# Optimization experiments

Hardware: AMD Instinct MI355X
Metric: run time of the kernel (lower is better)

Reference implementation:

```python
import jax, jax.numpy as jnp
import numpy as np

N_NODES = 100000
N_EDGES = 1000000
M_DIM = 4
HID = 64
N_GRAPHS = 64


def setup_inputs() -> dict:
    key = jax.random.key(0)
    ks = jax.random.split(key, 16)
    x = jax.random.normal(ks[0], (N_NODES, 1, M_DIM), dtype=jnp.float32)
    edge_index = jax.random.randint(ks[1], (2, N_EDGES), 0, N_NODES, dtype=jnp.int64)
    batch = jnp.sort(jax.random.randint(ks[2], (N_NODES,), 0, N_GRAPHS, dtype=jnp.int64))
    def lin(k, out_c, in_c):
        bound = 1.0 / np.sqrt(in_c)
        return jax.random.uniform(k, (out_c, in_c), jnp.float32, -bound, bound)
    inp = {"x": x, "edge_index": edge_index, "batch": batch}
    inp["W1l"] = lin(ks[3], HID, 1); inp["b1l"] = jnp.zeros((HID,), jnp.float32)
    inp["W1r"] = lin(ks[4], HID, 1)
    inp["W2l"] = lin(ks[5], HID, HID); inp["b2l"] = jnp.zeros((HID,), jnp.float32)
    inp["W2r"] = lin(ks[6], HID, HID)
    inp["W3l"] = lin(ks[7], HID, HID); inp["b3l"] = jnp.zeros((HID,), jnp.float32)
    inp["W3r"] = lin(ks[8], HID, HID)
    inp["Wlin"] = lin(ks[9], 1, HID); inp["blin"] = jnp.zeros((1,), jnp.float32)
    return inp


def _sage_conv(x, src, dst, Wl, bl, Wr):
    # x: [N, F, M]; mean aggregation over in-edges, then lin_l/lin_r GEMMs.
    N, F, M = x.shape
    msg = x[src]  # [E, F, M] gather
    s = jax.ops.segment_sum(msg, dst, num_segments=N)
    cnt = jax.ops.segment_sum(jnp.ones((src.shape[0],), x.dtype), dst, num_segments=N)
    agg = s / jnp.maximum(cnt, 1.0)[:, None, None]  # [N, F, M]
    C = Wl.shape[0]
    # torch .view(N*M, F) on contiguous [N,F,M] == row-major reshape (mixes F and M)
    h = (agg.reshape(N * M, F) @ Wl.T + bl).reshape(N, C, M)
    h = h + (x.reshape(N * M, F) @ Wr.T).reshape(N, C, M)
    return h


def reference(x, edge_index, batch, W1l, b1l, W1r, W2l, b2l, W2r, W3l, b3l, W3r, Wlin, blin):
    src, dst = edge_index[0], edge_index[1]
    h = jax.nn.relu(_sage_conv(x, src, dst, W1l, b1l, W1r))
    h = jax.nn.relu(_sage_conv(h, src, dst, W2l, b2l, W2r))
    h = jax.nn.relu(_sage_conv(h, src, dst, W3l, b3l, W3r))
    # new_global_mean_pool: scatter-mean over nodes -> [B, HID, M]
    sums = jax.ops.segment_sum(h, batch, num_segments=N_GRAPHS)
    cnts = jax.ops.segment_sum(jnp.ones((h.shape[0],), h.dtype), batch, num_segments=N_GRAPHS)
    pooled = sums / jnp.maximum(cnts, 1.0)[:, None, None]
    # dropout in eval mode == identity
    B, F, M = pooled.shape
    z = (pooled.reshape(B * M, F) @ Wlin.T + blin).reshape(B, M)
    return jax.nn.sigmoid(z).mean(axis=1)  # [B]
```

## Files before the change

### kernel.cpp

```cpp
#include <hip/hip_runtime.h>
#include <math.h>

#define TPB 256

typedef unsigned short ushort_t;
typedef unsigned char uchar_t;
typedef __attribute__((ext_vector_type(8))) short short8v;
typedef __attribute__((ext_vector_type(4))) float f32x4;
typedef __attribute__((ext_vector_type(8))) unsigned short ushort8;

__device__ __forceinline__ unsigned short f2b(float f) {
  union { float f; unsigned int i; } c; c.f = f;
  unsigned int x = c.i;
  x += 0x7FFFu + ((x >> 16) & 1u);
  return (unsigned short)(x >> 16);
}
__device__ __forceinline__ float b2f(unsigned short u) {
  union { unsigned int i; float f; } c; c.i = ((unsigned int)u) << 16; return c.f;
}

__device__ __forceinline__ short8v fp8x8_to_bf16(const uchar_t* p) {
  uint2 u = *(const uint2*)p;
  auto p0 = __builtin_amdgcn_cvt_pk_f32_fp8(u.x, false);
  auto p1 = __builtin_amdgcn_cvt_pk_f32_fp8(u.x, true);
  auto p2 = __builtin_amdgcn_cvt_pk_f32_fp8(u.y, false);
  auto p3 = __builtin_amdgcn_cvt_pk_f32_fp8(u.y, true);
  ushort8 o;
  o[0] = f2b(p0[0]); o[1] = f2b(p0[1]); o[2] = f2b(p1[0]); o[3] = f2b(p1[1]);
  o[4] = f2b(p2[0]); o[5] = f2b(p2[1]); o[6] = f2b(p3[0]); o[7] = f2b(p3[1]);
  union { ushort8 a; short8v b; } c; c.a = o; return c.b;
}

__global__ void k_histg(const int* __restrict__ dst, int* deg,
                        const int* __restrict__ batch, int* gcnt, int E, int N) {
  int t = blockIdx.x * TPB + threadIdx.x;
  if (t < E) atomicAdd(&deg[dst[t]], 1);
  int n0 = t * 16;
  if (n0 < N) {
    int n1 = min(n0 + 16, N);
    int cur = batch[n0];
    int c = 0;
    for (int n = n0; n < n1; ++n) {
      int b = batch[n];
      if (b != cur) { atomicAdd(&gcnt[cur], c); cur = b; c = 0; }
      ++c;
    }
    atomicAdd(&gcnt[cur], c);
  }
}

__global__ void k_scan1(const int* __restrict__ deg, int* rp, int* bsum, int N) {
  __shared__ int s[TPB];
  int t = threadIdx.x;
  int i = blockIdx.x * TPB + t;
  int v = (i < N) ? ((deg[i] + 7) & ~7) : 0;
  s[t] = v;
  __syncthreads();
  for (int d = 1; d < TPB; d <<= 1) {
    int u = (t >= d) ? s[t - d] : 0;
    __syncthreads();
    s[t] += u;
    __syncthreads();
  }
  if (i < N) rp[i] = s[t] - v;
  if (t == TPB - 1) bsum[blockIdx.x] = s[t];
}

__global__ void k_scan2(const int* bsum, int* boff, int nb) {
  __shared__ int s[1024];
  int t = threadIdx.x;
  int v = (t < nb) ? bsum[t] : 0;
  s[t] = v;
  __syncthreads();
  for (int d = 1; d < 1024; d <<= 1) {
    int u = (t >= d) ? s[t - d] : 0;
    __syncthreads();
    s[t] += u;
    __syncthreads();
  }
  if (t < nb) boff[t] = s[t] - v;
}

__global__ void k_scan3(int* rp, const int* __restrict__ boff, const int* __restrict__ bsum,
                        int* cursor, int N, int nb) {
  int i = blockIdx.x * TPB + threadIdx.x;
  if (i < N) {
    int v = rp[i] + boff[i >> 8];
    rp[i] = v;
    cursor[i] = v;
  } else if (i == N) {
    rp[N] = boff[nb - 1] + bsum[nb - 1];
  }
}

__global__ void k_fill(const int* __restrict__ src, const int* __restrict__ dst,
                       int* cursor, int* __restrict__ csr, int E) {
  int e = blockIdx.x * TPB + threadIdx.x;
  if (e < E) {
    int p = atomicAdd(&cursor[dst[e]], 1);
    csr[p] = src[e];
  }
}

__global__ void k_cvtw(const float* __restrict__ s0, const float* __restrict__ s1,
                       const float* __restrict__ s2, const float* __restrict__ s3,
                       ushort_t* d0, ushort_t* d1, ushort_t* d2, ushort_t* d3,
                       uchar_t* zr0, uchar_t* zr1, int n) {
  int i = blockIdx.x * TPB + threadIdx.x;
  if (i < n) { d0[i] = f2b(s0[i]); d1[i] = f2b(s1[i]); d2[i] = f2b(s2[i]); d3[i] = f2b(s3[i]); }
  if (blockIdx.x == 0) {
    if (threadIdx.x < 64) ((int*)zr0)[threadIdx.x] = 0;
    else if (threadIdx.x < 128) ((int*)zr1)[threadIdx.x - 64] = 0;
  }
}

__global__ void k_agg1(const float4* __restrict__ x, const int* __restrict__ rp,
                       const int* __restrict__ deg, const int* __restrict__ cursor,
                       int* __restrict__ csr, float4* __restrict__ agg1, int N) {
  int n = blockIdx.x * TPB + threadIdx.x;
  if (n >= N) return;
  int b = rp[n], e = rp[n + 1];
  float4 a = make_float4(0.f, 0.f, 0.f, 0.f);
  for (int i = b; i < e; i += 8) {
    int4 c0 = *(const int4*)(csr + i);
    int4 c1 = *(const int4*)(csr + i + 4);
    int id[8] = {c0.x, c0.y, c0.z, c0.w, c1.x, c1.y, c1.z, c1.w};
#pragma unroll
    for (int j = 0; j < 8; ++j) {
      unsigned idx = min((unsigned)id[j], (unsigned)(N - 1));
      float m = ((unsigned)id[j] < (unsigned)N) ? 1.f : 0.f;
      float4 v = x[idx];
      a.x += v.x * m; a.y += v.y * m; a.z += v.z * m; a.w += v.w * m;
    }
  }
  int d = deg[n];
  float inv = (d > 0) ? 1.f / (float)d : 0.f;
  a.x *= inv; a.y *= inv; a.z *= inv; a.w *= inv;
  agg1[n] = a;
  int c = cursor[n];
  for (int p2 = c; p2 < e; ++p2) csr[p2] = N;
}

__global__ void k_l1(const float* __restrict__ x, const float* __restrict__ agg1,
                     const float* __restrict__ W1l, const float* __restrict__ b1l,
                     const float* __restrict__ W1r, uchar_t* __restrict__ h8, int rows) {
  int q = blockIdx.x * TPB + threadIdx.x;
  if (q >= rows * 8) return;
  int r = q >> 3, c8 = (q & 7) * 8;
  float a = agg1[r], xx = x[r];
  float vv[8];
#pragma unroll
  for (int k = 0; k < 8; ++k)
    vv[k] = fmaxf(a * W1l[c8 + k] + b1l[c8 + k] + xx * W1r[c8 + k], 0.f);
  unsigned int w0 = __builtin_amdgcn_cvt_pk_fp8_f32(vv[0], vv[1], 0u, false);
  w0 = __builtin_amdgcn_cvt_pk_fp8_f32(vv[2], vv[3], w0, true);
  unsigned int w1 = __builtin_amdgcn_cvt_pk_fp8_f32(vv[4], vv[5], 0u, false);
  w1 = __builtin_amdgcn_cvt_pk_fp8_f32(vv[6], vv[7], w1, true);
  uint2 st; st.x = w0; st.y = w1;
  *(uint2*)(h8 + (size_t)r * 64 + c8) = st;
}

#define NB8(ACC, IDX) { \
    uint4 v = *(const uint4*)(h8sl + ((size_t)(unsigned)(IDX) << 8)); \
    auto q0 = __builtin_amdgcn_cvt_pk_f32_fp8(v.x, false); \
    auto q1 = __builtin_amdgcn_cvt_pk_f32_fp8(v.x, true);  \
    auto q2 = __builtin_amdgcn_cvt_pk_f32_fp8(v.y, false); \
    auto q3 = __builtin_amdgcn_cvt_pk_f32_fp8(v.y, true);  \
    auto q4 = __builtin_amdgcn_cvt_pk_f32_fp8(v.z, false); \
    auto q5 = __builtin_amdgcn_cvt_pk_f32_fp8(v.z, true);  \
    auto q6 = __builtin_amdgcn_cvt_pk_f32_fp8(v.w, false); \
    auto q7 = __builtin_amdgcn_cvt_pk_f32_fp8(v.w, true);  \
    ACC[0] += q0[0];  ACC[1] += q0[1];  ACC[2] += q1[0];  ACC[3] += q1[1];  \
    ACC[4] += q2[0];  ACC[5] += q2[1];  ACC[6] += q3[0];  ACC[7] += q3[1];  \
    ACC[8] += q4[0];  ACC[9] += q4[1];  ACC[10] += q5[0]; ACC[11] += q5[1]; \
    ACC[12] += q6[0]; ACC[13] += q6[1]; ACC[14] += q7[0]; ACC[15] += q7[1]; }

__global__ __launch_bounds__(256) void k_layer(
    const uchar_t* __restrict__ hIn8,
    const int* __restrict__ rp, const int* __restrict__ deg, const int* __restrict__ csr,
    const ushort_t* __restrict__ Wlb, const ushort_t* __restrict__ Wrb,
    const float* __restrict__ bias,
    uchar_t* __restrict__ hOut8, float* __restrict__ pooled,
    const int* __restrict__ batch, int N) {
  __shared__ ushort_t As[8192];
  int t = threadIdx.x;
  int wave = t >> 6, lane = t & 63;
  int g = lane >> 4, l15 = lane & 15;
  int gq = t >> 4, li = t & 15;
  int n0 = blockIdx.x * 32;
  int r0 = blockIdx.x * 128;

  const uchar_t* h8sl = hIn8 + li * 16;

  for (int k2 = 0; k2 < 2; ++k2) {
    int n = n0 + gq * 2 + k2;
    int b = rp[n], e = rp[n + 1];
    float acc[16];
#pragma unroll
    for (int j = 0; j < 16; ++j) acc[j] = 0.f;
    for (int i = b; i < e; i += 8) {
      int4 c0 = *(const int4*)(csr + i);
      int4 c1 = *(const int4*)(csr + i + 4);
      NB8(acc, c0.x) NB8(acc, c0.y) NB8(acc, c0.z) NB8(acc, c0.w)
      NB8(acc, c1.x) NB8(acc, c1.y) NB8(acc, c1.z) NB8(acc, c1.w)
    }
    int d = deg[n];
    float inv = (d > 0) ? 1.f / (float)d : 0.f;
    ushort8 pk0, pk1;
#pragma unroll
    for (int j = 0; j < 8; ++j) {
      pk0[j] = f2b(acc[j] * inv);
      pk1[j] = f2b(acc[j + 8] * inv);
    }
    int nl = gq * 2 + k2;
    int row = nl * 4 + (li >> 2);
    int cb = (li & 3) * 32;
    int xr = (row & 7) << 4;
    *(ushort8*)((char*)As + row * 128 + (cb ^ xr)) = pk0;
    *(ushort8*)((char*)As + row * 128 + ((cb + 16) ^ xr)) = pk1;
  }
  __syncthreads();

  short8v af[2][2], hf[2][2];
#pragma unroll
  for (int tile = 0; tile < 2; ++tile) {
    int arow = wave * 32 + tile * 16 + l15;
    int xr = (arow & 7) << 4;
    af[tile][0] = *(const short8v*)((char*)As + arow * 128 + ((g * 16) ^ xr));
    af[tile][1] = *(const short8v*)((char*)As + arow * 128 + ((g * 16 + 64) ^ xr));
    const uchar_t* hrow8 = hIn8 + (size_t)(r0 + arow) * 64;
    hf[tile][0] = fp8x8_to_bf16(hrow8 + g * 8);
    hf[tile][1] = fp8x8_to_bf16(hrow8 + 32 + g * 8);
  }

  f32x4 fac[4][2];
#pragma unroll
  for (int c = 0; c < 4; ++c) {
    float bv = bias[c * 16 + l15];
    const ushort_t* wl = Wlb + (size_t)(c * 16 + l15) * 64;
    const ushort_t* wr = Wrb + (size_t)(c * 16 + l15) * 64;
    short8v bl0 = *(const short8v*)(wl + g * 8);
    short8v bl1 = *(const short8v*)(wl + 32 + g * 8);
    short8v br0 = *(const short8v*)(wr + g * 8);
    short8v br1 = *(const short8v*)(wr + 32 + g * 8);
#pragma unroll
    for (int tile = 0; tile < 2; ++tile) {
      fac[c][tile] = (f32x4){bv, bv, bv, bv};
      fac[c][tile] = __builtin_amdgcn_mfma_f32_16x16x32_bf16(af[tile][0], bl0, fac[c][tile], 0, 0, 0);
      fac[c][tile] = __builtin_amdgcn_mfma_f32_16x16x32_bf16(af[tile][1], bl1, fac[c][tile], 0, 0, 0);
      fac[c][tile] = __builtin_amdgcn_mfma_f32_16x16x32_bf16(hf[tile][0], br0, fac[c][tile], 0, 0, 0);
      fac[c][tile] = __builtin_amdgcn_mfma_f32_16x16x32_bf16(hf[tile][1], br1, fac[c][tile], 0, 0, 0);
    }
  }

  if (hOut8) {
#pragma unroll
    for (int tile = 0; tile < 2; ++tile)
#pragma unroll
      for (int c = 0; c < 4; ++c)
#pragma unroll
        for (int i2 = 0; i2 < 4; ++i2) {
          int grow = r0 + wave * 32 + tile * 16 + g * 4 + i2;
          float v = fmaxf(fac[c][tile][i2], 0.f);
          hOut8[(size_t)grow * 64 + c * 16 + l15] =
              (uchar_t)(__builtin_amdgcn_cvt_pk_fp8_f32(v, v, 0u, false) & 0xFF);
        }
  } else {
    int bF = batch[n0], bL = batch[n0 + 31];
    if (bF == bL) {
      float* pool_s = (float*)As;
      __syncthreads();
      float vv[4][4];
#pragma unroll
      for (int c = 0; c < 4; ++c)
#pragma unroll
        for (int i2 = 0; i2 < 4; ++i2) {
          float v = fmaxf(fac[c][0][i2], 0.f) + fmaxf(fac[c][1][i2], 0.f);
          v += __shfl_xor(v, 16);
          v += __shfl_xor(v, 32);
          vv[c][i2] = v;
        }
      if (g == 0) {
#pragma unroll
        for (int c = 0; c < 4; ++c)
#pragma unroll
          for (int i2 = 0; i2 < 4; ++i2)
            pool_s[wave * 256 + i2 * 64 + c * 16 + l15] = vv[c][i2];
      }
      __syncthreads();
      float s = pool_s[t] + pool_s[256 + t] + pool_s[512 + t] + pool_s[768 + t];
      atomicAdd(&pooled[bF * 256 + t], s);
    } else {
#pragma unroll
      for (int tile = 0; tile < 2; ++tile)
#pragma unroll
        for (int c = 0; c < 4; ++c)
#pragma unroll
          for (int i2 = 0; i2 < 4; ++i2) {
            int grow = r0 + wave * 32 + tile * 16 + g * 4 + i2;
            int nn = grow >> 2;
            atomicAdd(&pooled[batch[nn] * 256 + (grow & 3) * 64 + c * 16 + l15],
                      fmaxf(fac[c][tile][i2], 0.f));
          }
    }
  }
}

__global__ void k_final(const float* __restrict__ pooled, const int* __restrict__ gcnt,
                        const float* __restrict__ Wlin, const float* __restrict__ blin,
                        float* __restrict__ out, int B) {
  int t = blockIdx.x * TPB + threadIdx.x;
  int b = t >> 2, j = t & 3;
  if (b >= B) return;
  float inv = 1.f / fmaxf((float)gcnt[b], 1.f);
  float s = blin[0];
  const float* p = pooled + b * 256 + j * 64;
#pragma unroll
  for (int f = 0; f < 64; ++f) s += p[f] * inv * Wlin[f];
  float z = 1.f / (1.f + expf(-s));
  z += __shfl_xor(z, 1);
  z += __shfl_xor(z, 2);
  if (j == 0) out[b] = 0.25f * z;
}

extern "C" void kernel_launch(void* const* d_in, const int* in_sizes, int n_in,
                              void* d_out, int out_size, void* d_ws, size_t ws_size,
                              hipStream_t stream) {
  const float* x   = (const float*)d_in[0];
  const int* edge  = (const int*)d_in[1];
  const int* batch = (const int*)d_in[2];
  const float* W1l = (const float*)d_in[3];
  const float* b1l = (const float*)d_in[4];
  const float* W1r = (const float*)d_in[5];
  const float* W2l = (const float*)d_in[6];
  const float* b2l = (const float*)d_in[7];
  const float* W2r = (const float*)d_in[8];
  const float* W3l = (const float*)d_in[9];
  const float* b3l = (const float*)d_in[10];
  const float* W3r = (const float*)d_in[11];
  const float* Wlin = (const float*)d_in[12];
  const float* blin = (const float*)d_in[13];
  float* out = (float*)d_out;

  const int N = in_sizes[0] / 4;
  const int E = in_sizes[1] / 2;
  const int B = out_size;
  const int rows = 4 * N;

  const int* srcA = edge;
  const int* dstA = edge + E;

  char* p = (char*)d_ws;
  auto carve = [&](size_t bytes) -> void* {
    void* r = (void*)p;
    p += (bytes + 255) & ~(size_t)255;
    return r;
  };
  char* zstart = p;
  int* deg     = (int*)carve((size_t)N * 4);
  int* gcnt    = (int*)carve((size_t)B * 4);
  float* pooled = (float*)carve((size_t)B * 256 * 4);
  size_t zlen  = (size_t)(p - zstart);
  int* rp      = (int*)carve((size_t)(N + 1) * 4);
  int* cursor  = (int*)carve((size_t)N * 4);
  int* bsum    = (int*)carve(4096);
  int* boff    = (int*)carve(4096);
  int* csr     = (int*)carve(((size_t)E + 8 * (size_t)N) * 4);
  float* agg1  = (float*)carve((size_t)N * 4 * 4);
  ushort_t* Wb2l = (ushort_t*)carve(4096 * 2);
  ushort_t* Wb2r = (ushort_t*)carve(4096 * 2);
  ushort_t* Wb3l = (ushort_t*)carve(4096 * 2);
  ushort_t* Wb3r = (ushort_t*)carve(4096 * 2);
  uchar_t* hA8  = (uchar_t*)carve(((size_t)N + 1) * 256);
  uchar_t* hB8  = (uchar_t*)carve(((size_t)N + 1) * 256);
  (void)ws_size; (void)n_in;

  hipMemsetAsync(zstart, 0, zlen, stream);

  int nbScan = (N + TPB - 1) / TPB;

  k_histg<<<(E + TPB - 1) / TPB, TPB, 0, stream>>>(dstA, deg, batch, gcnt, E, N);
  k_cvtw<<<16, TPB, 0, stream>>>(W2l, W2r, W3l, W3r, Wb2l, Wb2r, Wb3l, Wb3r,
                                 hA8 + (size_t)N * 256, hB8 + (size_t)N * 256, 4096);
  k_scan1<<<nbScan, TPB, 0, stream>>>(deg, rp, bsum, N);
  k_scan2<<<1, 1024, 0, stream>>>(bsum, boff, nbScan);
  k_scan3<<<(N + 1 + TPB - 1) / TPB, TPB, 0, stream>>>(rp, boff, bsum, cursor, N, nbScan);
  k_fill<<<(E + TPB - 1) / TPB, TPB, 0, stream>>>(srcA, dstA, cursor, csr, E);

  k_agg1<<<(N + TPB - 1) / TPB, TPB, 0, stream>>>((const float4*)x, rp, deg, cursor,
                                                  csr, (float4*)agg1, N);
  k_l1<<<((size_t)rows * 8 + TPB - 1) / TPB, TPB, 0, stream>>>(x, agg1, W1l, b1l, W1r, hA8, rows);

  int nbLayer = (N + 31) / 32;
  k_layer<<<nbLayer, TPB, 0, stream>>>(hA8, rp, deg, csr, Wb2l, Wb2r, b2l,
                                       hB8, (float*)nullptr, batch, N);
  k_layer<<<nbLayer, TPB, 0, stream>>>(hB8, rp, deg, csr, Wb3l, Wb3r, b3l,
                                       (uchar_t*)nullptr, pooled, batch, N);

  k_final<<<(B * 4 + TPB - 1) / TPB, TPB, 0, stream>>>(pooled, gcnt, Wlin, blin, out, B);
}
```

Measured before the change: 361.3 us.

## Use 512-thread layer blocks with one node per 16-lane group and 16-wide CSR padding

Result: slower. 415.0 us (+14.8%).

```diff
diff --git a/kernel.cpp b/kernel.cpp
--- a/kernel.cpp
+++ b/kernel.cpp
@@ -14,9 +14,6 @@
   unsigned int x = c.i;
   x += 0x7FFFu + ((x >> 16) & 1u);
   return (unsigned short)(x >> 16);
-}
-__device__ __forceinline__ float b2f(unsigned short u) {
-  union { unsigned int i; float f; } c; c.i = ((unsigned int)u) << 16; return c.f;
 }
 
 __device__ __forceinline__ short8v fp8x8_to_bf16(const uchar_t* p) {
@@ -53,7 +50,7 @@
   __shared__ int s[TPB];
   int t = threadIdx.x;
   int i = blockIdx.x * TPB + t;
-  int v = (i < N) ? ((deg[i] + 7) & ~7) : 0;
+  int v = (i < N) ? ((deg[i] + 15) & ~15) : 0;
   s[t] = v;
   __syncthreads();
   for (int d = 1; d < TPB; d <<= 1) {
@@ -175,7 +172,7 @@
     ACC[8] += q4[0];  ACC[9] += q4[1];  ACC[10] += q5[0]; ACC[11] += q5[1]; \
     ACC[12] += q6[0]; ACC[13] += q6[1]; ACC[14] += q7[0]; ACC[15] += q7[1]; }
 
-__global__ __launch_bounds__(256) void k_layer(
+__global__ __launch_bounds__(512) void k_layer(
     const uchar_t* __restrict__ hIn8,
     const int* __restrict__ rp, const int* __restrict__ deg, const int* __restrict__ csr,
     const ushort_t* __restrict__ Wlb, const ushort_t* __restrict__ Wrb,
@@ -192,17 +189,21 @@
 
   const uchar_t* h8sl = hIn8 + li * 16;
 
-  for (int k2 = 0; k2 < 2; ++k2) {
-    int n = n0 + gq * 2 + k2;
+  {
+    int n = n0 + gq;
     int b = rp[n], e = rp[n + 1];
     float acc[16];
 #pragma unroll
     for (int j = 0; j < 16; ++j) acc[j] = 0.f;
-    for (int i = b; i < e; i += 8) {
+    for (int i = b; i < e; i += 16) {
       int4 c0 = *(const int4*)(csr + i);
       int4 c1 = *(const int4*)(csr + i + 4);
+      int4 c2 = *(const int4*)(csr + i + 8);
+      int4 c3 = *(const int4*)(csr + i + 12);
       NB8(acc, c0.x) NB8(acc, c0.y) NB8(acc, c0.z) NB8(acc, c0.w)
       NB8(acc, c1.x) NB8(acc, c1.y) NB8(acc, c1.z) NB8(acc, c1.w)
+      NB8(acc, c2.x) NB8(acc, c2.y) NB8(acc, c2.z) NB8(acc, c2.w)
+      NB8(acc, c3.x) NB8(acc, c3.y) NB8(acc, c3.z) NB8(acc, c3.w)
     }
     int d = deg[n];
     float inv = (d > 0) ? 1.f / (float)d : 0.f;
@@ -212,8 +213,7 @@
       pk0[j] = f2b(acc[j] * inv);
       pk1[j] = f2b(acc[j + 8] * inv);
     }
-    int nl = gq * 2 + k2;
-    int row = nl * 4 + (li >> 2);
+    int row = gq * 4 + (li >> 2);
     int cb = (li & 3) * 32;
     int xr = (row & 7) << 4;
     *(ushort8*)((char*)As + row * 128 + (cb ^ xr)) = pk0;
@@ -221,19 +221,18 @@
   }
   __syncthreads();
 
-  short8v af[2][2], hf[2][2];
-#pragma unroll
-  for (int tile = 0; tile < 2; ++tile) {
-    int arow = wave * 32 + tile * 16 + l15;
+  short8v af0, af1, hf0, hf1;
+  {
+    int arow = wave * 16 + l15;
     int xr = (arow & 7) << 4;
-    af[tile][0] = *(const short8v*)((char*)As + arow * 128 + ((g * 16) ^ xr));
-    af[tile][1] = *(const short8v*)((char*)As + arow * 128 + ((g * 16 + 64) ^ xr));
+    af0 = *(const short8v*)((char*)As + arow * 128 + ((g * 16) ^ xr));
+    af1 = *(const short8v*)((char*)As + arow * 128 + ((g * 16 + 64) ^ xr));
     const uchar_t* hrow8 = hIn8 + (size_t)(r0 + arow) * 64;
-    hf[tile][0] = fp8x8_to_bf16(hrow8 + g * 8);
-    hf[tile][1] = fp8x8_to_bf16(hrow8 + 32 + g * 8);
-  }
-
-  f32x4 fac[4][2];
+    hf0 = fp8x8_to_bf16(hrow8 + g * 8);
+    hf1 = fp8x8_to_bf16(hrow8 + 32 + g * 8);
+  }
+
+  f32x4 fac[4];
 #pragma unroll
   for (int c = 0; c < 4; ++c) {
     float bv = bias[c * 16 + l15];
@@ -243,28 +242,23 @@
     short8v bl1 = *(const short8v*)(wl + 32 + g * 8);
     short8v br0 = *(const short8v*)(wr + g * 8);
     short8v br1 = *(const short8v*)(wr + 32 + g * 8);
-#pragma unroll
-    for (int tile = 0; tile < 2; ++tile) {
-      fac[c][tile] = (f32x4){bv, bv, bv, bv};
-      fac[c][tile] = __builtin_amdgcn_mfma_f32_16x16x32_bf16(af[tile][0], bl0, fac[c][tile], 0, 0, 0);
-      fac[c][tile] = __builtin_amdgcn_mfma_f32_16x16x32_bf16(af[tile][1], bl1, fac[c][tile], 0, 0, 0);
-      fac[c][tile] = __builtin_amdgcn_mfma_f32_16x16x32_bf16(hf[tile][0], br0, fac[c][tile], 0, 0, 0);
-      fac[c][tile] = __builtin_amdgcn_mfma_f32_16x16x32_bf16(hf[tile][1], br1, fac[c][tile], 0, 0, 0);
-    }
+    fac[c] = (f32x4){bv, bv, bv, bv};
+    fac[c] = __builtin_amdgcn_mfma_f32_16x16x32_bf16(af0, bl0, fac[c], 0, 0, 0);
+    fac[c] = __builtin_amdgcn_mfma_f32_16x16x32_bf16(af1, bl1, fac[c], 0, 0, 0);
+    fac[c] = __builtin_amdgcn_mfma_f32_16x16x32_bf16(hf0, br0, fac[c], 0, 0, 0);
+    fac[c] = __builtin_amdgcn_mfma_f32_16x16x32_bf16(hf1, br1, fac[c], 0, 0, 0);
   }
 
   if (hOut8) {
 #pragma unroll
-    for (int tile = 0; tile < 2; ++tile)
-#pragma unroll
-      for (int c = 0; c < 4; ++c)
-#pragma unroll
-        for (int i2 = 0; i2 < 4; ++i2) {
-          int grow = r0 + wave * 32 + tile * 16 + g * 4 + i2;
-          float v = fmaxf(fac[c][tile][i2], 0.f);
-          hOut8[(size_t)grow * 64 + c * 16 + l15] =
-              (uchar_t)(__builtin_amdgcn_cvt_pk_fp8_f32(v, v, 0u, false) & 0xFF);
-        }
+    for (int c = 0; c < 4; ++c)
+#pragma unroll
+      for (int i2 = 0; i2 < 4; ++i2) {
+        int grow = r0 + wave * 16 + g * 4 + i2;
+        float v = fmaxf(fac[c][i2], 0.f);
+        hOut8[(size_t)grow * 64 + c * 16 + l15] =
+            (uchar_t)(__builtin_amdgcn_cvt_pk_fp8_f32(v, v, 0u, false) & 0xFF);
+      }
   } else {
     int bF = batch[n0], bL = batch[n0 + 31];
     if (bF == bL) {
@@ -275,7 +269,7 @@
       for (int c = 0; c < 4; ++c)
 #pragma unroll
         for (int i2 = 0; i2 < 4; ++i2) {
-          float v = fmaxf(fac[c][0][i2], 0.f) + fmaxf(fac[c][1][i2], 0.f);
+          float v = fmaxf(fac[c][i2], 0.f);
           v += __shfl_xor(v, 16);
           v += __shfl_xor(v, 32);
           vv[c][i2] = v;
@@ -288,20 +282,22 @@
             pool_s[wave * 256 + i2 * 64 + c * 16 + l15] = vv[c][i2];
       }
       __syncthreads();
-      float s = pool_s[t] + pool_s[256 + t] + pool_s[512 + t] + pool_s[768 + t];
-      atomicAdd(&pooled[bF * 256 + t], s);
+      if (t < 256) {
+        float s = 0.f;
+#pragma unroll
+        for (int w = 0; w < 8; ++w) s += pool_s[w * 256 + t];
+        atomicAdd(&pooled[bF * 256 + t], s);
+      }
     } else {
 #pragma unroll
-      for (int tile = 0; tile < 2; ++tile)
-#pragma unroll
-        for (int c = 0; c < 4; ++c)
-#pragma unroll
-          for (int i2 = 0; i2 < 4; ++i2) {
-            int grow = r0 + wave * 32 + tile * 16 + g * 4 + i2;
-            int nn = grow >> 2;
-            atomicAdd(&pooled[batch[nn] * 256 + (grow & 3) * 64 + c * 16 + l15],
-                      fmaxf(fac[c][tile][i2], 0.f));
-          }
+      for (int c = 0; c < 4; ++c)
+#pragma unroll
+        for (int i2 = 0; i2 < 4; ++i2) {
+          int grow = r0 + wave * 16 + g * 4 + i2;
+          int nn = grow >> 2;
+          atomicAdd(&pooled[batch[nn] * 256 + (grow & 3) * 64 + c * 16 + l15],
+                    fmaxf(fac[c][i2], 0.f));
+        }
     }
   }
 }
@@ -365,7 +361,7 @@
   int* cursor  = (int*)carve((size_t)N * 4);
   int* bsum    = (int*)carve(4096);
   int* boff    = (int*)carve(4096);
-  int* csr     = (int*)carve(((size_t)E + 8 * (size_t)N) * 4);
+  int* csr     = (int*)carve(((size_t)E + 16 * (size_t)N) * 4);
   float* agg1  = (float*)carve((size_t)N * 4 * 4);
   ushort_t* Wb2l = (ushort_t*)carve(4096 * 2);
   ushort_t* Wb2r = (ushort_t*)carve(4096 * 2);
@@ -392,9 +388,9 @@
   k_l1<<<((size_t)rows * 8 + TPB - 1) / TPB, TPB, 0, stream>>>(x, agg1, W1l, b1l, W1r, hA8, rows);
 
   int nbLayer = (N + 31) / 32;
-  k_layer<<<nbLayer, TPB, 0, stream>>>(hA8, rp, deg, csr, Wb2l, Wb2r, b2l,
+  k_layer<<<nbLayer, 512, 0, stream>>>(hA8, rp, deg, csr, Wb2l, Wb2r, b2l,
                                        hB8, (float*)nullptr, batch, N);
-  k_layer<<<nbLayer, TPB, 0, stream>>>(hB8, rp, deg, csr, Wb3l, Wb3r, b3l,
+  k_layer<<<nbLayer, 512, 0, stream>>>(hB8, rp, deg, csr, Wb3l, Wb3r, b3l,
                                        (uchar_t*)nullptr, pooled, batch, N);
 
   k_final<<<(B * 4 + TPB - 1) / TPB, TPB, 0, stream>>>(pooled, gcnt, Wlin, blin, out, B);
```

## Apply linear transform before neighbor aggregation and split layers into GEMM and gather

Applied to the files above, without the earlier changes.

Result: slower. 393.1 us (+8.8%).

```diff
diff --git a/kernel.cpp b/kernel.cpp
--- a/kernel.cpp
+++ b/kernel.cpp
@@ -14,9 +14,6 @@
   unsigned int x = c.i;
   x += 0x7FFFu + ((x >> 16) & 1u);
   return (unsigned short)(x >> 16);
-}
-__device__ __forceinline__ float b2f(unsigned short u) {
-  union { unsigned int i; float f; } c; c.i = ((unsigned int)u) << 16; return c.f;
 }
 
 __device__ __forceinline__ short8v fp8x8_to_bf16(const uchar_t* p) {
@@ -105,13 +102,10 @@
 __global__ void k_cvtw(const float* __restrict__ s0, const float* __restrict__ s1,
                        const float* __restrict__ s2, const float* __restrict__ s3,
                        ushort_t* d0, ushort_t* d1, ushort_t* d2, ushort_t* d3,
-                       uchar_t* zr0, uchar_t* zr1, int n) {
+                       uchar_t* zr0, int n) {
   int i = blockIdx.x * TPB + threadIdx.x;
   if (i < n) { d0[i] = f2b(s0[i]); d1[i] = f2b(s1[i]); d2[i] = f2b(s2[i]); d3[i] = f2b(s3[i]); }
-  if (blockIdx.x == 0) {
-    if (threadIdx.x < 64) ((int*)zr0)[threadIdx.x] = 0;
-    else if (threadIdx.x < 128) ((int*)zr1)[threadIdx.x - 64] = 0;
-  }
+  if (blockIdx.x == 0 && threadIdx.x < 64) ((int*)zr0)[threadIdx.x] = 0;
 }
 
 __global__ void k_agg1(const float4* __restrict__ x, const int* __restrict__ rp,
@@ -141,169 +135,156 @@
   for (int p2 = c; p2 < e; ++p2) csr[p2] = N;
 }
 
-__global__ void k_l1(const float* __restrict__ x, const float* __restrict__ agg1,
-                     const float* __restrict__ W1l, const float* __restrict__ b1l,
-                     const float* __restrict__ W1r, uchar_t* __restrict__ h8, int rows) {
-  int q = blockIdx.x * TPB + threadIdx.x;
-  if (q >= rows * 8) return;
-  int r = q >> 3, c8 = (q & 7) * 8;
-  float a = agg1[r], xx = x[r];
-  float vv[8];
-#pragma unroll
-  for (int k = 0; k < 8; ++k)
-    vv[k] = fmaxf(a * W1l[c8 + k] + b1l[c8 + k] + xx * W1r[c8 + k], 0.f);
-  unsigned int w0 = __builtin_amdgcn_cvt_pk_fp8_f32(vv[0], vv[1], 0u, false);
-  w0 = __builtin_amdgcn_cvt_pk_fp8_f32(vv[2], vv[3], w0, true);
-  unsigned int w1 = __builtin_amdgcn_cvt_pk_fp8_f32(vv[4], vv[5], 0u, false);
-  w1 = __builtin_amdgcn_cvt_pk_fp8_f32(vv[6], vv[7], w1, true);
-  uint2 st; st.x = w0; st.y = w1;
-  *(uint2*)(h8 + (size_t)r * 64 + c8) = st;
-}
-
-#define NB8(ACC, IDX) { \
-    uint4 v = *(const uint4*)(h8sl + ((size_t)(unsigned)(IDX) << 8)); \
-    auto q0 = __builtin_amdgcn_cvt_pk_f32_fp8(v.x, false); \
-    auto q1 = __builtin_amdgcn_cvt_pk_f32_fp8(v.x, true);  \
-    auto q2 = __builtin_amdgcn_cvt_pk_f32_fp8(v.y, false); \
-    auto q3 = __builtin_amdgcn_cvt_pk_f32_fp8(v.y, true);  \
-    auto q4 = __builtin_amdgcn_cvt_pk_f32_fp8(v.z, false); \
-    auto q5 = __builtin_amdgcn_cvt_pk_f32_fp8(v.z, true);  \
-    auto q6 = __builtin_amdgcn_cvt_pk_f32_fp8(v.w, false); \
-    auto q7 = __builtin_amdgcn_cvt_pk_f32_fp8(v.w, true);  \
-    ACC[0] += q0[0];  ACC[1] += q0[1];  ACC[2] += q1[0];  ACC[3] += q1[1];  \
-    ACC[4] += q2[0];  ACC[5] += q2[1];  ACC[6] += q3[0];  ACC[7] += q3[1];  \
-    ACC[8] += q4[0];  ACC[9] += q4[1];  ACC[10] += q5[0]; ACC[11] += q5[1]; \
-    ACC[12] += q6[0]; ACC[13] += q6[1]; ACC[14] += q7[0]; ACC[15] += q7[1]; }
-
-__global__ __launch_bounds__(256) void k_layer(
+__global__ __launch_bounds__(256) void k_gemm(
     const uchar_t* __restrict__ hIn8,
-    const int* __restrict__ rp, const int* __restrict__ deg, const int* __restrict__ csr,
+    const float* __restrict__ xf, const float* __restrict__ agg1f,
+    const float* __restrict__ W1l, const float* __restrict__ b1l,
+    const float* __restrict__ W1r,
     const ushort_t* __restrict__ Wlb, const ushort_t* __restrict__ Wrb,
     const float* __restrict__ bias,
-    uchar_t* __restrict__ hOut8, float* __restrict__ pooled,
-    const int* __restrict__ batch, int N) {
-  __shared__ ushort_t As[8192];
+    uchar_t* __restrict__ Yl8, uchar_t* __restrict__ Yr8, int rows) {
   int t = threadIdx.x;
   int wave = t >> 6, lane = t & 63;
   int g = lane >> 4, l15 = lane & 15;
-  int gq = t >> 4, li = t & 15;
-  int n0 = blockIdx.x * 32;
-  int r0 = blockIdx.x * 128;
-
-  const uchar_t* h8sl = hIn8 + li * 16;
-
-  for (int k2 = 0; k2 < 2; ++k2) {
-    int n = n0 + gq * 2 + k2;
-    int b = rp[n], e = rp[n + 1];
-    float acc[16];
-#pragma unroll
-    for (int j = 0; j < 16; ++j) acc[j] = 0.f;
-    for (int i = b; i < e; i += 8) {
-      int4 c0 = *(const int4*)(csr + i);
-      int4 c1 = *(const int4*)(csr + i + 4);
-      NB8(acc, c0.x) NB8(acc, c0.y) NB8(acc, c0.z) NB8(acc, c0.w)
-      NB8(acc, c1.x) NB8(acc, c1.y) NB8(acc, c1.z) NB8(acc, c1.w)
-    }
-    int d = deg[n];
-    float inv = (d > 0) ? 1.f / (float)d : 0.f;
-    ushort8 pk0, pk1;
-#pragma unroll
-    for (int j = 0; j < 8; ++j) {
-      pk0[j] = f2b(acc[j] * inv);
-      pk1[j] = f2b(acc[j + 8] * inv);
-    }
-    int nl = gq * 2 + k2;
-    int row = nl * 4 + (li >> 2);
-    int cb = (li & 3) * 32;
-    int xr = (row & 7) << 4;
-    *(ushort8*)((char*)As + row * 128 + (cb ^ xr)) = pk0;
-    *(ushort8*)((char*)As + row * 128 + ((cb + 16) ^ xr)) = pk1;
-  }
-  __syncthreads();
-
-  short8v af[2][2], hf[2][2];
-#pragma unroll
-  for (int tile = 0; tile < 2; ++tile) {
-    int arow = wave * 32 + tile * 16 + l15;
-    int xr = (arow & 7) << 4;
-    af[tile][0] = *(const short8v*)((char*)As + arow * 128 + ((g * 16) ^ xr));
-    af[tile][1] = *(const short8v*)((char*)As + arow * 128 + ((g * 16 + 64) ^ xr));
-    const uchar_t* hrow8 = hIn8 + (size_t)(r0 + arow) * 64;
-    hf[tile][0] = fp8x8_to_bf16(hrow8 + g * 8);
-    hf[tile][1] = fp8x8_to_bf16(hrow8 + 32 + g * 8);
-  }
-
-  f32x4 fac[4][2];
+  int r0 = blockIdx.x * 64 + wave * 16;
+  int r = r0 + l15;
+
+  short8v af0, af1;
+  if (hIn8) {
+    const uchar_t* hrow = hIn8 + (size_t)r * 64;
+    af0 = fp8x8_to_bf16(hrow + g * 8);
+    af1 = fp8x8_to_bf16(hrow + 32 + g * 8);
+  } else {
+    float sA = agg1f[r], sX = xf[r];
+    ushort8 o0, o1;
+#pragma unroll
+    for (int k = 0; k < 8; ++k) {
+      int c0 = g * 8 + k, c1 = 32 + g * 8 + k;
+      o0[k] = f2b(fmaxf(sA * W1l[c0] + b1l[c0] + sX * W1r[c0], 0.f));
+      o1[k] = f2b(fmaxf(sA * W1l[c1] + b1l[c1] + sX * W1r[c1], 0.f));
+    }
+    union { ushort8 a; short8v b; } u0, u1;
+    u0.a = o0; u1.a = o1;
+    af0 = u0.b; af1 = u1.b;
+  }
+
 #pragma unroll
   for (int c = 0; c < 4; ++c) {
-    float bv = bias[c * 16 + l15];
     const ushort_t* wl = Wlb + (size_t)(c * 16 + l15) * 64;
     const ushort_t* wr = Wrb + (size_t)(c * 16 + l15) * 64;
     short8v bl0 = *(const short8v*)(wl + g * 8);
     short8v bl1 = *(const short8v*)(wl + 32 + g * 8);
     short8v br0 = *(const short8v*)(wr + g * 8);
     short8v br1 = *(const short8v*)(wr + 32 + g * 8);
-#pragma unroll
-    for (int tile = 0; tile < 2; ++tile) {
-      fac[c][tile] = (f32x4){bv, bv, bv, bv};
-      fac[c][tile] = __builtin_amdgcn_mfma_f32_16x16x32_bf16(af[tile][0], bl0, fac[c][tile], 0, 0, 0);
-      fac[c][tile] = __builtin_amdgcn_mfma_f32_16x16x32_bf16(af[tile][1], bl1, fac[c][tile], 0, 0, 0);
-      fac[c][tile] = __builtin_amdgcn_mfma_f32_16x16x32_bf16(hf[tile][0], br0, fac[c][tile], 0, 0, 0);
-      fac[c][tile] = __builtin_amdgcn_mfma_f32_16x16x32_bf16(hf[tile][1], br1, fac[c][tile], 0, 0, 0);
-    }
-  }
-
-  if (hOut8) {
-#pragma unroll
-    for (int tile = 0; tile < 2; ++tile)
-#pragma unroll
-      for (int c = 0; c < 4; ++c)
-#pragma unroll
-        for (int i2 = 0; i2 < 4; ++i2) {
-          int grow = r0 + wave * 32 + tile * 16 + g * 4 + i2;
-          float v = fmaxf(fac[c][tile][i2], 0.f);
-          hOut8[(size_t)grow * 64 + c * 16 + l15] =
-              (uchar_t)(__builtin_amdgcn_cvt_pk_fp8_f32(v, v, 0u, false) & 0xFF);
-        }
-  } else {
-    int bF = batch[n0], bL = batch[n0 + 31];
-    if (bF == bL) {
-      float* pool_s = (float*)As;
-      __syncthreads();
-      float vv[4][4];
-#pragma unroll
-      for (int c = 0; c < 4; ++c)
-#pragma unroll
-        for (int i2 = 0; i2 < 4; ++i2) {
-          float v = fmaxf(fac[c][0][i2], 0.f) + fmaxf(fac[c][1][i2], 0.f);
-          v += __shfl_xor(v, 16);
-          v += __shfl_xor(v, 32);
-          vv[c][i2] = v;
-        }
-      if (g == 0) {
-#pragma unroll
-        for (int c = 0; c < 4; ++c)
-#pragma unroll
-          for (int i2 = 0; i2 < 4; ++i2)
-            pool_s[wave * 256 + i2 * 64 + c * 16 + l15] = vv[c][i2];
+    float bv = bias[c * 16 + l15];
+    f32x4 accl = (f32x4){0.f, 0.f, 0.f, 0.f};
+    f32x4 accr = (f32x4){bv, bv, bv, bv};
+    accl = __builtin_amdgcn_mfma_f32_16x16x32_bf16(af0, bl0, accl, 0, 0, 0);
+    accl = __builtin_amdgcn_mfma_f32_16x16x32_bf16(af1, bl1, accl, 0, 0, 0);
+    accr = __builtin_amdgcn_mfma_f32_16x16x32_bf16(af0, br0, accr, 0, 0, 0);
+    accr = __builtin_amdgcn_mfma_f32_16x16x32_bf16(af1, br1, accr, 0, 0, 0);
+#pragma unroll
+    for (int i = 0; i < 4; ++i) {
+      size_t off = (size_t)(r0 + g * 4 + i) * 64 + c * 16 + l15;
+      Yl8[off] = (uchar_t)(__builtin_amdgcn_cvt_pk_fp8_f32(accl[i], accl[i], 0u, false) & 0xFF);
+      Yr8[off] = (uchar_t)(__builtin_amdgcn_cvt_pk_fp8_f32(accr[i], accr[i], 0u, false) & 0xFF);
+    }
+  }
+}
+
+#define ADD8(IDX) { \
+    uint2 v = *(const uint2*)(base + ((size_t)(unsigned)(IDX) << 8)); \
+    auto q0 = __builtin_amdgcn_cvt_pk_f32_fp8(v.x, false); \
+    auto q1 = __builtin_amdgcn_cvt_pk_f32_fp8(v.x, true);  \
+    auto q2 = __builtin_amdgcn_cvt_pk_f32_fp8(v.y, false); \
+    auto q3 = __builtin_amdgcn_cvt_pk_f32_fp8(v.y, true);  \
+    acc[0] += q0[0]; acc[1] += q0[1]; acc[2] += q1[0]; acc[3] += q1[1]; \
+    acc[4] += q2[0]; acc[5] += q2[1]; acc[6] += q3[0]; acc[7] += q3[1]; }
+
+__global__ __launch_bounds__(256) void k_gather(
+    const uchar_t* __restrict__ Yl8, const uchar_t* __restrict__ Yr8,
+    const int* __restrict__ rp, const int* __restrict__ deg, const int* __restrict__ csr,
+    uchar_t* __restrict__ hOut8, int N) {
+  int tid = blockIdx.x * TPB + threadIdx.x;
+  int n = tid >> 5, s = tid & 31;
+  if (n >= N) return;
+  int b = rp[n], e = rp[n + 1];
+  const uchar_t* base = Yl8 + s * 8;
+
+  float acc[8];
+#pragma unroll
+  for (int j = 0; j < 8; ++j) acc[j] = 0.f;
+
+  for (int i = b; i < e; i += 8) {
+    int4 c0 = *(const int4*)(csr + i);
+    int4 c1 = *(const int4*)(csr + i + 4);
+    ADD8(c0.x) ADD8(c0.y) ADD8(c0.z) ADD8(c0.w)
+    ADD8(c1.x) ADD8(c1.y) ADD8(c1.z) ADD8(c1.w)
+  }
+
+  int d = deg[n];
+  float inv = (d > 0) ? 1.f / (float)d : 0.f;
+  uint2 yr = *(const uint2*)(Yr8 + (size_t)n * 256 + s * 8);
+  auto y0 = __builtin_amdgcn_cvt_pk_f32_fp8(yr.x, false);
+  auto y1 = __builtin_amdgcn_cvt_pk_f32_fp8(yr.x, true);
+  auto y2 = __builtin_amdgcn_cvt_pk_f32_fp8(yr.y, false);
+  auto y3 = __builtin_amdgcn_cvt_pk_f32_fp8(yr.y, true);
+  float h0 = fmaxf(acc[0] * inv + y0[0], 0.f);
+  float h1 = fmaxf(acc[1] * inv + y0[1], 0.f);
+  float h2 = fmaxf(acc[2] * inv + y1[0], 0.f);
+  float h3 = fmaxf(acc[3] * inv + y1[1], 0.f);
+  float h4 = fmaxf(acc[4] * inv + y2[0], 0.f);
+  float h5 = fmaxf(acc[5] * inv + y2[1], 0.f);
+  float h6 = fmaxf(acc[6] * inv + y3[0], 0.f);
+  float h7 = fmaxf(acc[7] * inv + y3[1], 0.f);
+  unsigned int w0 = __builtin_amdgcn_cvt_pk_fp8_f32(h0, h1, 0u, false);
+  w0 = __builtin_amdgcn_cvt_pk_fp8_f32(h2, h3, w0, true);
+  unsigned int w1 = __builtin_amdgcn_cvt_pk_fp8_f32(h4, h5, 0u, false);
+  w1 = __builtin_amdgcn_cvt_pk_fp8_f32(h6, h7, w1, true);
+  uint2 st; st.x = w0; st.y = w1;
+  *(uint2*)(hOut8 + (size_t)n * 256 + s * 8) = st;
+}
+
+__device__ __forceinline__ float fp8_to_f32(uchar_t u) {
+  return __builtin_amdgcn_cvt_pk_f32_fp8((unsigned int)u, false)[0];
+}
+
+__global__ void k_pool(const uchar_t* __restrict__ h, const int* __restrict__ batch,
+                       float* pooled, int N) {
+  int t = threadIdx.x;
+  int nPer = (N + gridDim.x - 1) / gridDim.x;
+  int n0 = blockIdx.x * nPer;
+  int n1 = min(N, n0 + nPer);
+  if (n0 >= n1) return;
+  float acc = 0.f;
+  int cur = batch[n0];
+  int n = n0;
+  for (; n + 3 < n1; n += 4) {
+    int b0 = batch[n], b3 = batch[n + 3];
+    float v0 = fp8_to_f32(h[(size_t)n * 256 + t]);
+    float v1 = fp8_to_f32(h[(size_t)(n + 1) * 256 + t]);
+    float v2 = fp8_to_f32(h[(size_t)(n + 2) * 256 + t]);
+    float v3 = fp8_to_f32(h[(size_t)(n + 3) * 256 + t]);
+    if (b0 == b3) {
+      if (b0 != cur) { atomicAdd(&pooled[cur * 256 + t], acc); acc = 0.f; cur = b0; }
+      acc += (v0 + v1) + (v2 + v3);
+    } else {
+      int bb1 = batch[n + 1], bb2 = batch[n + 2];
+      int bb[4] = {b0, bb1, bb2, b3};
+      float vv[4] = {v0, v1, v2, v3};
+#pragma unroll
+      for (int j = 0; j < 4; ++j) {
+        if (bb[j] != cur) { atomicAdd(&pooled[cur * 256 + t], acc); acc = 0.f; cur = bb[j]; }
+        acc += vv[j];
       }
-      __syncthreads();
-      float s = pool_s[t] + pool_s[256 + t] + pool_s[512 + t] + pool_s[768 + t];
-      atomicAdd(&pooled[bF * 256 + t], s);
-    } else {
-#pragma unroll
-      for (int tile = 0; tile < 2; ++tile)
-#pragma unroll
-        for (int c = 0; c < 4; ++c)
-#pragma unroll
-          for (int i2 = 0; i2 < 4; ++i2) {
-            int grow = r0 + wave * 32 + tile * 16 + g * 4 + i2;
-            int nn = grow >> 2;
-            atomicAdd(&pooled[batch[nn] * 256 + (grow & 3) * 64 + c * 16 + l15],
-                      fmaxf(fac[c][tile][i2], 0.f));
-          }
-    }
-  }
+    }
+  }
+  for (; n < n1; ++n) {
+    int b = batch[n];
+    if (b != cur) { atomicAdd(&pooled[cur * 256 + t], acc); acc = 0.f; cur = b; }
+    acc += fp8_to_f32(h[(size_t)n * 256 + t]);
+  }
+  atomicAdd(&pooled[cur * 256 + t], acc);
 }
 
 __global__ void k_final(const float* __restrict__ pooled, const int* __restrict__ gcnt,
@@ -371,8 +352,9 @@
   ushort_t* Wb2r = (ushort_t*)carve(4096 * 2);
   ushort_t* Wb3l = (ushort_t*)carve(4096 * 2);
   ushort_t* Wb3r = (ushort_t*)carve(4096 * 2);
-  uchar_t* hA8  = (uchar_t*)carve(((size_t)N + 1) * 256);
-  uchar_t* hB8  = (uchar_t*)carve(((size_t)N + 1) * 256);
+  uchar_t* Yl8 = (uchar_t*)carve(((size_t)N + 1) * 256);
+  uchar_t* Yr8 = (uchar_t*)carve((size_t)N * 256);
+  uchar_t* h8  = (uchar_t*)carve((size_t)N * 256);
   (void)ws_size; (void)n_in;
 
   hipMemsetAsync(zstart, 0, zlen, stream);
@@ -381,7 +363,7 @@
 
   k_histg<<<(E + TPB - 1) / TPB, TPB, 0, stream>>>(dstA, deg, batch, gcnt, E, N);
   k_cvtw<<<16, TPB, 0, stream>>>(W2l, W2r, W3l, W3r, Wb2l, Wb2r, Wb3l, Wb3r,
-                                 hA8 + (size_t)N * 256, hB8 + (size_t)N * 256, 4096);
+                                 Yl8 + (size_t)N * 256, 4096);
   k_scan1<<<nbScan, TPB, 0, stream>>>(deg, rp, bsum, N);
   k_scan2<<<1, 1024, 0, stream>>>(bsum, boff, nbScan);
   k_scan3<<<(N + 1 + TPB - 1) / TPB, TPB, 0, stream>>>(rp, boff, bsum, cursor, N, nbScan);
@@ -389,13 +371,18 @@
 
   k_agg1<<<(N + TPB - 1) / TPB, TPB, 0, stream>>>((const float4*)x, rp, deg, cursor,
                                                   csr, (float4*)agg1, N);
-  k_l1<<<((size_t)rows * 8 + TPB - 1) / TPB, TPB, 0, stream>>>(x, agg1, W1l, b1l, W1r, hA8, rows);
-
-  int nbLayer = (N + 31) / 32;
-  k_layer<<<nbLayer, TPB, 0, stream>>>(hA8, rp, deg, csr, Wb2l, Wb2r, b2l,
-                                       hB8, (float*)nullptr, batch, N);
-  k_layer<<<nbLayer, TPB, 0, stream>>>(hB8, rp, deg, csr, Wb3l, Wb3r, b3l,
-                                       (uchar_t*)nullptr, pooled, batch, N);
-
+
+  int nbGemm = (rows + 63) / 64;
+  int nbGather = ((size_t)N * 32 + TPB - 1) / TPB;
+
+  k_gemm<<<nbGemm, TPB, 0, stream>>>((const uchar_t*)nullptr, x, agg1, W1l, b1l, W1r,
+                                     Wb2l, Wb2r, b2l, Yl8, Yr8, rows);
+  k_gather<<<nbGather, TPB, 0, stream>>>(Yl8, Yr8, rp, deg, csr, h8, N);
+
+  k_gemm<<<nbGemm, TPB, 0, stream>>>(h8, x, agg1, W1l, b1l, W1r,
+                                     Wb3l, Wb3r, b3l, Yl8, Yr8, rows);
+  k_gather<<<nbGather, TPB, 0, stream>>>(Yl8, Yr8, rp, deg, csr, h8, N);
+
+  k_pool<<<1024, TPB, 0, stream>>>(h8, batch, pooled, N);
   k_final<<<(B * 4 + TPB - 1) / TPB, TPB, 0, stream>>>(pooled, gcnt, Wlin, blin, out, B);
 }
```
